# Performance work log

Hardware: AMD Instinct MI355X
Metric: run time of the kernel (lower is better)

## Reference

```python
import math
import jax
import jax.numpy as jnp
import numpy as np

N_IMG = 8
A = 3
H = 100
W = 100
STRIDE = 16
IMG = 1600
PRE_NMS_TOP_N = 2000
POST_NMS_TOP_N = 1000
NMS_THRESH = 0.7
MIN_SIZE = 0
BBOX_XFORM_CLIP = math.log(1000.0 / 16.0)


def setup_inputs() -> dict:
    key = jax.random.key(0)
    k1, k2 = jax.random.split(key)
    objectness = jax.random.normal(k1, (N_IMG, A, H, W), jnp.float32)
    box_regression = jax.random.normal(k2, (N_IMG, A * 4, H, W), jnp.float32) * 0.5
    # Grid anchors, flattened in (H, W, A) order to match objectness.permute(0,2,3,1)
    cy = (jnp.arange(H, dtype=jnp.float32) + 0.5) * STRIDE  # [H]
    cx = (jnp.arange(W, dtype=jnp.float32) + 0.5) * STRIDE  # [W]
    half = jnp.array([64.0, 128.0, 256.0], jnp.float32) / 2.0  # [A]
    cy = cy[:, None, None]  # [H,1,1]
    cx = cx[None, :, None]  # [1,W,1]
    s = half[None, None, :]  # [1,1,A]
    x1, y1, x2, y2 = jnp.broadcast_arrays(cx - s, cy - s, cx + s, cy + s)
    anc = jnp.stack([x1, y1, x2, y2], axis=-1).reshape(-1, 4)  # [H*W*A, 4]
    anchors = jnp.broadcast_to(anc[None], (N_IMG, H * W * A, 4)).copy()
    return {
        "objectness": objectness,
        "box_regression": box_regression,
        "anchors": anchors,
        "image_height": IMG,
        "image_width": IMG,
    }


def _decode(deltas, boxes):
    # BoxCoder(weights=(1,1,1,1)).decode with TO_REMOVE=1
    widths = boxes[..., 2] - boxes[..., 0] + 1.0
    heights = boxes[..., 3] - boxes[..., 1] + 1.0
    ctr_x = boxes[..., 0] + 0.5 * widths
    ctr_y = boxes[..., 1] + 0.5 * heights
    dx, dy = deltas[..., 0], deltas[..., 1]
    dw = jnp.minimum(deltas[..., 2], BBOX_XFORM_CLIP)
    dh = jnp.minimum(deltas[..., 3], BBOX_XFORM_CLIP)
    pcx = dx * widths + ctr_x
    pcy = dy * heights + ctr_y
    pw = jnp.exp(dw) * widths
    ph = jnp.exp(dh) * heights
    return jnp.stack(
        [pcx - 0.5 * pw, pcy - 0.5 * ph, pcx + 0.5 * pw - 1.0, pcy + 0.5 * ph - 1.0],
        axis=-1,
    )


def _nms_keep(boxes, valid, thresh):
    # boxes [n,4] sorted by descending score; valid: pre-filter mask.
    n = boxes.shape[0]
    x1, y1, x2, y2 = boxes[:, 0], boxes[:, 1], boxes[:, 2], boxes[:, 3]
    areas = (x2 - x1 + 1.0) * (y2 - y1 + 1.0)
    xx1 = jnp.maximum(x1[:, None], x1[None, :])
    yy1 = jnp.maximum(y1[:, None], y1[None, :])
    xx2 = jnp.minimum(x2[:, None], x2[None, :])
    yy2 = jnp.minimum(y2[:, None], y2[None, :])
    inter = jnp.maximum(xx2 - xx1 + 1.0, 0.0) * jnp.maximum(yy2 - yy1 + 1.0, 0.0)
    iou = inter / (areas[:, None] + areas[None, :] - inter)
    idx = jnp.arange(n)

    def body(i, keep):
        sup = keep[i] & (iou[i] > thresh) & (idx > i)
        return keep & ~sup

    return jax.lax.fori_loop(0, n, body, valid)


def _forward(objectness, box_regression, anchors, image_height, image_width):
    N, A_, H_, W_ = objectness.shape
    scores = jax.nn.sigmoid(objectness.transpose(0, 2, 3, 1).reshape(N, -1))  # [N, A*H*W]
    deltas = (
        box_regression.reshape(N, A_, 4, H_, W_)
        .transpose(0, 3, 4, 1, 2)
        .reshape(N, -1, 4)
    )
    pre = min(PRE_NMS_TOP_N, scores.shape[1])
    top_scores, top_idx = jax.lax.top_k(scores, pre)  # sorted descending
    deltas = jnp.take_along_axis(deltas, top_idx[:, :, None], axis=1)
    anc = jnp.take_along_axis(anchors, top_idx[:, :, None], axis=1)
    props = _decode(deltas, anc)  # [N, pre, 4]
    # clip to image (fact = 1)
    xs = jnp.clip(props[..., 0::2], 0.0, image_width - 1.0)
    ys = jnp.clip(props[..., 1::2], 0.0, image_height - 1.0)
    props = jnp.stack([xs[..., 0], ys[..., 0], xs[..., 1], ys[..., 1]], axis=-1)
    # filter small / out-of-image-center boxes
    ws = props[..., 2] - props[..., 0] + 1.0
    hs = props[..., 3] - props[..., 1] + 1.0
    xc = props[..., 0] + ws / 2.0
    yc = props[..., 1] + hs / 2.0
    valid = (ws >= MIN_SIZE) & (hs >= MIN_SIZE) & (xc < image_width) & (yc < image_height)
    keep = jax.vmap(lambda b, v: _nms_keep(b, v, NMS_THRESH))(props, valid)

    def _select(b, s, k):
        # compact kept boxes (already score-sorted) into fixed-size output
        rank = jnp.cumsum(k) - 1
        tgt = jnp.where(k & (rank < POST_NMS_TOP_N), rank, POST_NMS_TOP_N)
        ob = jnp.zeros((POST_NMS_TOP_N + 1, 4), b.dtype).at[tgt].set(b)[:POST_NMS_TOP_N]
        os = jnp.zeros((POST_NMS_TOP_N + 1,), s.dtype).at[tgt].set(s)[:POST_NMS_TOP_N]
        ov = jnp.arange(POST_NMS_TOP_N) < jnp.minimum(jnp.sum(k), POST_NMS_TOP_N)
        return ob, os, ov

    return jax.vmap(_select)(props, top_scores, keep)


def reference(objectness, box_regression, anchors, image_height, image_width):
    # Returns (boxes [N,post,4], objectness scores [N,post], valid mask [N,post])
    return _forward(objectness, box_regression, anchors, image_height, image_width)
```

## Files before the change

kernel.cpp:

```cpp
#include <hip/hip_runtime.h>
#include <math.h>
#include <stdint.h>

#define NIMG   8
#define NA     30000
#define PRE_N  2000
#define POST_N 1000
#define NMS_TH 0.7f
#define DCLIP  4.135166556742356f
#define IMGF   1600.0f
#define IMGM1  1599.0f
#define CAND_MAX 4096


__global__ __launch_bounds__(1024) void hist_compact(
    const float* __restrict__ obj,
    uint64_t* __restrict__ candBuf, unsigned int* __restrict__ candCnt)
{
    const int n    = blockIdx.x;
    const int tid  = threadIdx.x;
    const int lane = tid & 63;
    const int wid  = tid >> 6;

    __shared__ unsigned int hist[4096];
    __shared__ unsigned int wsum[16];
    __shared__ unsigned int scal[4];

    for (int b = tid; b < 4096; b += 1024) hist[b] = 0u;
    if (tid < 4) scal[tid] = 0u;
    __syncthreads();

    const float* objn = obj + n * NA;

    for (int j = tid; j < NA; j += 1024) {
        unsigned int u = __float_as_uint(objn[j]);
        unsigned int k = (u & 0x80000000u) ? ~u : (u | 0x80000000u);
        atomicAdd(&hist[k >> 20], 1u);
    }
    __syncthreads();

    unsigned int c0 = hist[tid*4+0], c1 = hist[tid*4+1],
                 c2 = hist[tid*4+2], c3 = hist[tid*4+3];
    unsigned int p = c0 + c1 + c2 + c3;
    unsigned int s = p;
    #pragma unroll
    for (int off = 1; off < 64; off <<= 1) {
        unsigned int v = __shfl_down(s, off);
        if (lane + off < 64) s += v;
    }
    if (lane == 0) wsum[wid] = s;
    __syncthreads();
    unsigned int wafter = 0;
    for (int w = wid + 1; w < 16; ++w) wafter += wsum[w];
    unsigned int after = (s - p) + wafter;
    {
        unsigned int S3 = after + c3;
        unsigned int S2 = S3 + c2;
        unsigned int S1 = S2 + c1;
        unsigned int S0 = S1 + c0;
        if (S3 >= PRE_N && after < PRE_N) { scal[2] = tid*4+3; }
        if (S2 >= PRE_N && S3    < PRE_N) { scal[2] = tid*4+2; }
        if (S1 >= PRE_N && S2    < PRE_N) { scal[2] = tid*4+1; }
        if (S0 >= PRE_N && S1    < PRE_N) { scal[2] = tid*4+0; }
    }
    __syncthreads();
    const unsigned int bstar = scal[2];

    for (int j = tid; j < NA; j += 1024) {
        unsigned int u = __float_as_uint(objn[j]);
        unsigned int k = (u & 0x80000000u) ? ~u : (u | 0x80000000u);
        if ((k >> 20) < bstar) continue;
        int a = j / 10000, t = j - a * 10000;
        uint64_t key = (((uint64_t)(~k)) << 32) | (unsigned int)(t * 3 + a);
        unsigned int pos = atomicAdd(&scal[0], 1u);
        if (pos < CAND_MAX) candBuf[n * CAND_MAX + pos] = key;
    }
    __syncthreads();
    if (tid == 0) candCnt[n] = min(scal[0], (unsigned int)CAND_MAX);
}

__global__ __launch_bounds__(64) void rank_decode(
    const float* __restrict__ breg,
    const uint64_t* __restrict__ candBuf, const unsigned int* __restrict__ candCnt,
    float* __restrict__ wsBoxes, float* __restrict__ wsScores,
    int* __restrict__ wsValid)
{
    const int n    = blockIdx.x >> 6;
    const int tile = blockIdx.x & 63;
    const int lane = threadIdx.x;

    const int C = (int)candCnt[n];
    if (tile * 64 >= C) return;

    const uint64_t* cb = candBuf + n * CAND_MAX;
    const int my = tile * 64 + lane;
    const uint64_t km = (my < C) ? cb[my] : ~0ull;

    unsigned int rank = 0;
    const int nch = (C + 63) >> 6;
    for (int ch = 0; ch < nch; ++ch) {
        const int j = ch * 64 + lane;
        uint64_t ck = (j < C) ? cb[j] : ~0ull;
        unsigned int clo = (unsigned int)ck, chi = (unsigned int)(ck >> 32);
        #pragma unroll
        for (int c = 0; c < 64; ++c) {
            unsigned int lo = (unsigned int)__builtin_amdgcn_readlane((int)clo, c);
            unsigned int hi = (unsigned int)__builtin_amdgcn_readlane((int)chi, c);
            uint64_t kc = ((uint64_t)hi << 32) | lo;
            rank += (kc < km) ? 1u : 0u;
        }
    }
    if (my >= C || rank >= PRE_N) return;

    unsigned int idx = (unsigned int)km;
    unsigned int k   = ~((unsigned int)(km >> 32));
    unsigned int u   = (k & 0x80000000u) ? (k & 0x7fffffffu) : ~k;
    float logit = __uint_as_float(u);
    float score = 1.0f / (1.0f + expf(-logit));

    int a = idx % 3, t = idx / 3, w = t % 100, h = t / 100;
    const float* bp = breg + n*120000 + (a*4)*10000 + t;
    float dx = bp[0], dy = bp[10000], dw = bp[20000], dh = bp[30000];

    float half = (a == 0) ? 32.0f : ((a == 1) ? 64.0f : 128.0f);
    float cx = w * 16.0f + 8.0f, cy = h * 16.0f + 8.0f;
    float x1 = cx - half, y1 = cy - half, x2 = cx + half, y2 = cy + half;
    float wd = x2 - x1 + 1.0f, hg = y2 - y1 + 1.0f;
    float cxr = x1 + 0.5f * wd, cyr = y1 + 0.5f * hg;
    dw = fminf(dw, DCLIP); dh = fminf(dh, DCLIP);
    float pcx = dx * wd + cxr, pcy = dy * hg + cyr;
    float pw = expf(dw) * wd, ph = expf(dh) * hg;
    float px1 = pcx - 0.5f * pw, py1 = pcy - 0.5f * ph;
    float px2 = pcx + 0.5f * pw - 1.0f, py2 = pcy + 0.5f * ph - 1.0f;
    px1 = fminf(fmaxf(px1, 0.0f), IMGM1);
    px2 = fminf(fmaxf(px2, 0.0f), IMGM1);
    py1 = fminf(fmaxf(py1, 0.0f), IMGM1);
    py2 = fminf(fmaxf(py2, 0.0f), IMGM1);
    float wss = px2 - px1 + 1.0f, hss = py2 - py1 + 1.0f;
    float xc = px1 + wss * 0.5f, yc = py1 + hss * 0.5f;
    int valid = (wss >= 0.0f) && (hss >= 0.0f) && (xc < IMGF) && (yc < IMGF);

    ((float4*)wsBoxes)[n * PRE_N + (int)rank] = make_float4(px1, py1, px2, py2);
    wsScores[n * PRE_N + (int)rank] = score;
    wsValid [n * PRE_N + (int)rank] = valid;
}

__global__ __launch_bounds__(512) void nms_mask(
    const float* __restrict__ wsBoxes, uint64_t* __restrict__ mask)
{
    const int blk  = blockIdx.x;
    const int n    = blk >> 5;
    const int i_t  = blk & 31;
    const int tid  = threadIdx.x;
    const int lane = tid & 63;
    const int wv   = tid >> 6;

    __shared__ uint64_t tile[64 * 33];

    for (int idx = tid; idx < 64 * 33; idx += 512) tile[idx] = 0ull;
    __syncthreads();

    const int r = i_t * 64 + lane;
    float4 rb = (r < PRE_N) ? ((const float4*)wsBoxes)[n * PRE_N + r]
                            : make_float4(0.f, 0.f, 0.f, 0.f);
    float ra = (rb.z - rb.x + 1.0f) * (rb.w - rb.y + 1.0f);

    for (int j_t = i_t + wv; j_t < 32; j_t += 8) {
        const int j = j_t * 64 + lane;
        float4 cb = (j < PRE_N) ? ((const float4*)wsBoxes)[n * PRE_N + j]
                                : make_float4(3e30f, 3e30f, 3e30f, 3e30f);
        float ca = (cb.z - cb.x + 1.0f) * (cb.w - cb.y + 1.0f);
        const uint64_t jmask = (j_t == 31) ? 0xFFFFull : ~0ull;
        const bool diag = (j_t == i_t);
        uint64_t myword = 0ull;

        #pragma unroll
        for (int c = 0; c < 64; ++c) {
            float rx1 = __int_as_float(__builtin_amdgcn_readlane(__float_as_int(rb.x), c));
            float ry1 = __int_as_float(__builtin_amdgcn_readlane(__float_as_int(rb.y), c));
            float rx2 = __int_as_float(__builtin_amdgcn_readlane(__float_as_int(rb.z), c));
            float ry2 = __int_as_float(__builtin_amdgcn_readlane(__float_as_int(rb.w), c));
            float rar = __int_as_float(__builtin_amdgcn_readlane(__float_as_int(ra), c));
            float xx1 = fmaxf(rx1, cb.x), yy1 = fmaxf(ry1, cb.y);
            float xx2 = fminf(rx2, cb.z), yy2 = fminf(ry2, cb.w);
            float ww = fmaxf(xx2 - xx1 + 1.0f, 0.0f);
            float hh = fmaxf(yy2 - yy1 + 1.0f, 0.0f);
            float inter = ww * hh;
            float denom = rar + ca - inter;
            unsigned long long bits = __ballot(inter > NMS_TH * denom) & jmask;
            if (diag) bits &= (c == 63) ? 0ull : ((~0ull) << (c + 1));
            if (lane == c) myword = bits;
        }
        tile[lane * 33 + j_t] = myword;
    }
    __syncthreads();

    uint64_t* mrow = mask + ((size_t)n * PRE_N + (size_t)i_t * 64) * 32;
    const int cmax = (i_t == 31) ? 16 : 64;
    for (int idx = tid; idx < cmax * 32; idx += 512) {
        const int rr = idx >> 5, w = idx & 31;
        mrow[idx] = tile[rr * 33 + w];
    }
}

#define SL(n,b) \
    "global_load_dword v" #n ", %[voff], %[sbase]\n\t" \
    "v_add_u32 %[voff], 0x100, %[voff]\n\t"

#define SS(n,b) \
    "s_waitcnt vmcnt(63)\n\t" \
    "v_readlane_b32 %[t], v" #n ", %[lw]\n\t" \
    "s_bitcmp1_b32 %[win], " #b "\n\t" \
    "s_cselect_b32 %[m], 0, -1\n\t" \
    "s_sub_i32 %[kept], %[kept], %[m]\n\t" \
    "s_and_b32 %[t], %[t], %[m]\n\t" \
    "s_or_b32 %[win], %[win], %[t]\n\t" \
    "v_and_b32 v" #n ", %[m], v" #n "\n\t" \
    "v_or_b32 %[rem], %[rem], v" #n "\n\t" \
    "global_load_dword v" #n ", %[voff], %[sbase]\n\t" \
    "v_add_u32 %[voff], 0x100, %[voff]\n\t"

#define SN(n,b,w) \
    "s_waitcnt vmcnt(" #w ")\n\t" \
    "v_readlane_b32 %[t], v" #n ", %[lw]\n\t" \
    "s_bitcmp1_b32 %[win], " #b "\n\t" \
    "s_cselect_b32 %[m], 0, -1\n\t" \
    "s_sub_i32 %[kept], %[kept], %[m]\n\t" \
    "s_and_b32 %[t], %[t], %[m]\n\t" \
    "s_or_b32 %[win], %[win], %[t]\n\t" \
    "v_and_b32 v" #n ", %[m], v" #n "\n\t" \
    "v_or_b32 %[rem], %[rem], v" #n "\n\t"

#define SWIN \
    "s_add_u32 %[lw], %[lw], 1\n\t" \
    "v_readlane_b32 %[t], %[rem], %[lw]\n\t" \
    "s_mov_b32 %[win], %[t]\n\t"

#define ROW_A(M) M(64,0) M(65,1) M(66,2) M(67,3) M(68,4) M(69,5) M(70,6) M(71,7) \
    M(72,8) M(73,9) M(74,10) M(75,11) M(76,12) M(77,13) M(78,14) M(79,15) \
    M(80,16) M(81,17) M(82,18) M(83,19) M(84,20) M(85,21) M(86,22) M(87,23) \
    M(88,24) M(89,25) M(90,26) M(91,27) M(92,28) M(93,29) M(94,30) M(95,31)
#define ROW_B(M) M(96,0) M(97,1) M(98,2) M(99,3) M(100,4) M(101,5) M(102,6) M(103,7) \
    M(104,8) M(105,9) M(106,10) M(107,11) M(108,12) M(109,13) M(110,14) M(111,15) \
    M(112,16) M(113,17) M(114,18) M(115,19) M(116,20) M(117,21) M(118,22) M(119,23) \
    M(120,24) M(121,25) M(122,26) M(123,27) M(124,28) M(125,29) M(126,30) M(127,31)

__global__ __launch_bounds__(256) void nms_scan_select(
    const float* __restrict__ wsBoxes, const float* __restrict__ wsScores,
    const int* __restrict__ wsValid, const uint64_t* __restrict__ mask,
    float* __restrict__ out)
{
    const int n   = blockIdx.x;
    const int tid = threadIdx.x;

    __shared__ __align__(8) unsigned char invb[256];
    __shared__ unsigned int keepw32[64];
    __shared__ int sscan[256];

    unsigned int byte = 0xFFu;
    if (tid < PRE_N / 8) {
        byte = 0u;
        for (int q = 0; q < 8; ++q)
            byte |= (wsValid[n * PRE_N + tid * 8 + q] ? 0u : 1u) << q;
    }
    invb[tid] = (unsigned char)byte;
    __syncthreads();

    if (tid < 64) {
        unsigned int rem = ((const unsigned int*)invb)[tid];
        unsigned long long sbase =
            (unsigned long long)(const void*)(mask + (size_t)n * PRE_N * 32);
        unsigned int voff = (unsigned int)(tid * 4);
        int win_, m_, t_, lw_, kept_, cnt_;

        asm volatile(
            "s_waitcnt vmcnt(0) lgkmcnt(0)\n\t"
            "s_mov_b32 %[kept], 0\n\t"
            "s_mov_b32 %[lw], 0\n\t"
            ROW_A(SL) ROW_B(SL)
            "v_readlane_b32 %[t], %[rem], %[lw]\n\t"
            "s_mov_b32 %[win], %[t]\n\t"
            "s_mov_b32 %[cnt], 30\n\t"
            "Lnms_%=:\n\t"
            ROW_A(SS)
            SWIN
            ROW_B(SS)
            SWIN
            "s_cmp_ge_i32 %[kept], 0x3e8\n\t"
            "s_cbranch_scc1 Lend_%=\n\t"
            "s_sub_u32 %[cnt], %[cnt], 1\n\t"
            "s_cmp_lg_u32 %[cnt], 0\n\t"
            "s_cbranch_scc1 Lnms_%=\n\t"
            SS(64,0) SS(65,1) SS(66,2) SS(67,3) SS(68,4) SS(69,5) SS(70,6) SS(71,7)
            SS(72,8) SS(73,9) SS(74,10) SS(75,11) SS(76,12) SS(77,13) SS(78,14) SS(79,15)
            SN(80,16,63) SN(81,17,62) SN(82,18,61) SN(83,19,60)
            SN(84,20,59) SN(85,21,58) SN(86,22,57) SN(87,23,56)
            SN(88,24,55) SN(89,25,54) SN(90,26,53) SN(91,27,52)
            SN(92,28,51) SN(93,29,50) SN(94,30,49) SN(95,31,48)
            SWIN
            SN(96,0,47) SN(97,1,46) SN(98,2,45) SN(99,3,44)
            SN(100,4,43) SN(101,5,42) SN(102,6,41) SN(103,7,40)
            SN(104,8,39) SN(105,9,38) SN(106,10,37) SN(107,11,36)
            SN(108,12,35) SN(109,13,34) SN(110,14,33) SN(111,15,32)
            SN(112,16,31) SN(113,17,30) SN(114,18,29) SN(115,19,28)
            SN(116,20,27) SN(117,21,26) SN(118,22,25) SN(119,23,24)
            SN(120,24,23) SN(121,25,22) SN(122,26,21) SN(123,27,20)
            SN(124,28,19) SN(125,29,18) SN(126,30,17) SN(127,31,16)
            SWIN
            SN(64,0,15) SN(65,1,14) SN(66,2,13) SN(67,3,12)
            SN(68,4,11) SN(69,5,10) SN(70,6,9) SN(71,7,8)
            SN(72,8,7) SN(73,9,6) SN(74,10,5) SN(75,11,4)
            SN(76,12,3) SN(77,13,2) SN(78,14,1) SN(79,15,0)
            "Lend_%=:\n\t"
            "s_waitcnt vmcnt(0)\n\t"
            : [rem]"+v"(rem), [voff]"+v"(voff),
              [win]"=&s"(win_), [m]"=&s"(m_), [t]"=&s"(t_),
              [lw]"=&s"(lw_), [kept]"=&s"(kept_), [cnt]"=&s"(cnt_)
            : [sbase]"s"(sbase)
            : "scc", "vcc", "memory",
              "v64","v65","v66","v67","v68","v69","v70","v71",
              "v72","v73","v74","v75","v76","v77","v78","v79",
              "v80","v81","v82","v83","v84","v85","v86","v87",
              "v88","v89","v90","v91","v92","v93","v94","v95",
              "v96","v97","v98","v99","v100","v101","v102","v103",
              "v104","v105","v106","v107","v108","v109","v110","v111",
              "v112","v113","v114","v115","v116","v117","v118","v119",
              "v120","v121","v122","v123","v124","v125","v126","v127");

        keepw32[tid] = ~rem;
    }
    __syncthreads();

    int c[8]; const int base8 = tid * 8;
    int lsum = 0;
    for (int q = 0; q < 8; ++q) {
        const int i = base8 + q;
        c[q] = (i < PRE_N) ? (int)((keepw32[i >> 5] >> (i & 31)) & 1u) : 0;
        lsum += c[q];
    }
    sscan[tid] = lsum;
    __syncthreads();
    for (int off = 1; off < 256; off <<= 1) {
        int v = (tid >= off) ? sscan[tid - off] : 0;
        __syncthreads();
        sscan[tid] += v;
        __syncthreads();
    }
    const int excl  = sscan[tid] - lsum;
    const int total = sscan[255];

    float* ob  = out + n * POST_N * 4;
    float* osc = out + NIMG * POST_N * 4 + n * POST_N;
    float* ovd = out + NIMG * POST_N * 5 + n * POST_N;

    for (int i = tid; i < POST_N * 4; i += 256) ob[i] = 0.0f;
    for (int i = tid; i < POST_N; i += 256) osc[i] = 0.0f;
    const int lim = min(total, POST_N);
    for (int i = tid; i < POST_N; i += 256) ovd[i] = (i < lim) ? 1.0f : 0.0f;
    __syncthreads();

    int run = excl;
    for (int q = 0; q < 8; ++q) {
        const int i = base8 + q;
        if (i < PRE_N && c[q]) {
            if (run < POST_N) {
                float4 b = ((const float4*)wsBoxes)[n * PRE_N + i];
                ob[run * 4 + 0] = b.x;
                ob[run * 4 + 1] = b.y;
                ob[run * 4 + 2] = b.z;
                ob[run * 4 + 3] = b.w;
                osc[run] = wsScores[n * PRE_N + i];
            }
            run++;
        }
    }
}

extern "C" void kernel_launch(void* const* d_in, const int* in_sizes, int n_in,
                              void* d_out, int out_size, void* d_ws, size_t ws_size,
                              hipStream_t stream) {
    const float* obj  = (const float*)d_in[0];
    const float* breg = (const float*)d_in[1];
    float* ws        = (float*)d_ws;
    float* wsBoxes   = ws;
    float* wsScores  = ws + 64000;
    int*   wsValid   = (int*)(ws + 80000);
    uint64_t* wsMask = (uint64_t*)(ws + 96000);
    uint64_t*     candBuf = wsMask;
    unsigned int* candCnt = (unsigned int*)(wsMask + NIMG * CAND_MAX);

    hist_compact<<<NIMG, 1024, 0, stream>>>(obj, candBuf, candCnt);
    rank_decode<<<NIMG * 64, 64, 0, stream>>>(breg, candBuf, candCnt,
                                              wsBoxes, wsScores, wsValid);
    nms_mask<<<NIMG * 32, 512, 0, stream>>>(wsBoxes, wsMask);
    nms_scan_select<<<NIMG, 256, 0, stream>>>(wsBoxes, wsScores, wsValid, wsMask,
                                              (float*)d_out);
}
```

Baseline: 185.0 us.

## Fuse top-k selection and decode into one kernel with bucketed ranking

Merges the histogram/compaction kernel and the rank/decode kernel into a single per-image kernel. Candidates are scattered into shared memory grouped by histogram bucket using suffix offsets, so each candidate's rank only needs comparisons within its own bucket instead of against all candidates. This removes a kernel launch, the global candidate buffer round trip, and the quadratic rank loop. In exchange, decode now runs on only 8 blocks, and large buckets could cause serial comparison loops.

```diff
diff --git a/kernel.cpp b/kernel.cpp
--- a/kernel.cpp
+++ b/kernel.cpp
@@ -13,21 +13,23 @@
 #define CAND_MAX 4096
 
 
-__global__ __launch_bounds__(1024) void hist_compact(
-    const float* __restrict__ obj,
-    uint64_t* __restrict__ candBuf, unsigned int* __restrict__ candCnt)
+__global__ __launch_bounds__(1024) void topk_decode(
+    const float* __restrict__ obj, const float* __restrict__ breg,
+    float* __restrict__ wsBoxes, float* __restrict__ wsScores,
+    int* __restrict__ wsValid)
 {
     const int n    = blockIdx.x;
     const int tid  = threadIdx.x;
     const int lane = tid & 63;
     const int wid  = tid >> 6;
 
-    __shared__ unsigned int hist[4096];
-    __shared__ unsigned int wsum[16];
-    __shared__ unsigned int scal[4];
+    __shared__ unsigned int   hist[4096];
+    __shared__ unsigned short sufx[4096];
+    __shared__ uint64_t       grp[CAND_MAX];
+    __shared__ unsigned int   wsum[16];
+    __shared__ unsigned int   sbstar;
 
     for (int b = tid; b < 4096; b += 1024) hist[b] = 0u;
-    if (tid < 4) scal[tid] = 0u;
     __syncthreads();
 
     const float* objn = obj + n * NA;
@@ -58,91 +60,79 @@
         unsigned int S2 = S3 + c2;
         unsigned int S1 = S2 + c1;
         unsigned int S0 = S1 + c0;
-        if (S3 >= PRE_N && after < PRE_N) { scal[2] = tid*4+3; }
-        if (S2 >= PRE_N && S3    < PRE_N) { scal[2] = tid*4+2; }
-        if (S1 >= PRE_N && S2    < PRE_N) { scal[2] = tid*4+1; }
-        if (S0 >= PRE_N && S1    < PRE_N) { scal[2] = tid*4+0; }
-    }
-    __syncthreads();
-    const unsigned int bstar = scal[2];
+        if (S3 >= PRE_N && after < PRE_N) { sbstar = tid*4+3; }
+        if (S2 >= PRE_N && S3    < PRE_N) { sbstar = tid*4+2; }
+        if (S1 >= PRE_N && S2    < PRE_N) { sbstar = tid*4+1; }
+        if (S0 >= PRE_N && S1    < PRE_N) { sbstar = tid*4+0; }
+        sufx[tid*4+0] = (unsigned short)S1;
+        sufx[tid*4+1] = (unsigned short)S2;
+        sufx[tid*4+2] = (unsigned short)S3;
+        sufx[tid*4+3] = (unsigned short)after;
+    }
+    hist[tid*4+0] = 0u; hist[tid*4+1] = 0u;
+    hist[tid*4+2] = 0u; hist[tid*4+3] = 0u;
+    __syncthreads();
+    const unsigned int bstar = sbstar;
 
     for (int j = tid; j < NA; j += 1024) {
         unsigned int u = __float_as_uint(objn[j]);
         unsigned int k = (u & 0x80000000u) ? ~u : (u | 0x80000000u);
-        if ((k >> 20) < bstar) continue;
+        unsigned int b = k >> 20;
+        if (b < bstar) continue;
         int a = j / 10000, t = j - a * 10000;
         uint64_t key = (((uint64_t)(~k)) << 32) | (unsigned int)(t * 3 + a);
-        unsigned int pos = atomicAdd(&scal[0], 1u);
-        if (pos < CAND_MAX) candBuf[n * CAND_MAX + pos] = key;
-    }
-    __syncthreads();
-    if (tid == 0) candCnt[n] = min(scal[0], (unsigned int)CAND_MAX);
-}
-
-__global__ __launch_bounds__(64) void rank_decode(
-    const float* __restrict__ breg,
-    const uint64_t* __restrict__ candBuf, const unsigned int* __restrict__ candCnt,
-    float* __restrict__ wsBoxes, float* __restrict__ wsScores,
-    int* __restrict__ wsValid)
-{
-    const int n    = blockIdx.x >> 6;
-    const int tile = blockIdx.x & 63;
-    const int lane = threadIdx.x;
-
-    const int C = (int)candCnt[n];
-    if (tile * 64 >= C) return;
-
-    const uint64_t* cb = candBuf + n * CAND_MAX;
-    const int my = tile * 64 + lane;
-    const uint64_t km = (my < C) ? cb[my] : ~0ull;
-
-    unsigned int rank = 0;
-    const int nch = (C + 63) >> 6;
-    for (int ch = 0; ch < nch; ++ch) {
-        const int j = ch * 64 + lane;
-        uint64_t ck = (j < C) ? cb[j] : ~0ull;
-        unsigned int clo = (unsigned int)ck, chi = (unsigned int)(ck >> 32);
-        #pragma unroll
-        for (int c = 0; c < 64; ++c) {
-            unsigned int lo = (unsigned int)__builtin_amdgcn_readlane((int)clo, c);
-            unsigned int hi = (unsigned int)__builtin_amdgcn_readlane((int)chi, c);
-            uint64_t kc = ((uint64_t)hi << 32) | lo;
-            rank += (kc < km) ? 1u : 0u;
-        }
-    }
-    if (my >= C || rank >= PRE_N) return;
-
-    unsigned int idx = (unsigned int)km;
-    unsigned int k   = ~((unsigned int)(km >> 32));
-    unsigned int u   = (k & 0x80000000u) ? (k & 0x7fffffffu) : ~k;
-    float logit = __uint_as_float(u);
-    float score = 1.0f / (1.0f + expf(-logit));
-
-    int a = idx % 3, t = idx / 3, w = t % 100, h = t / 100;
-    const float* bp = breg + n*120000 + (a*4)*10000 + t;
-    float dx = bp[0], dy = bp[10000], dw = bp[20000], dh = bp[30000];
-
-    float half = (a == 0) ? 32.0f : ((a == 1) ? 64.0f : 128.0f);
-    float cx = w * 16.0f + 8.0f, cy = h * 16.0f + 8.0f;
-    float x1 = cx - half, y1 = cy - half, x2 = cx + half, y2 = cy + half;
-    float wd = x2 - x1 + 1.0f, hg = y2 - y1 + 1.0f;
-    float cxr = x1 + 0.5f * wd, cyr = y1 + 0.5f * hg;
-    dw = fminf(dw, DCLIP); dh = fminf(dh, DCLIP);
-    float pcx = dx * wd + cxr, pcy = dy * hg + cyr;
-    float pw = expf(dw) * wd, ph = expf(dh) * hg;
-    float px1 = pcx - 0.5f * pw, py1 = pcy - 0.5f * ph;
-    float px2 = pcx + 0.5f * pw - 1.0f, py2 = pcy + 0.5f * ph - 1.0f;
-    px1 = fminf(fmaxf(px1, 0.0f), IMGM1);
-    px2 = fminf(fmaxf(px2, 0.0f), IMGM1);
-    py1 = fminf(fmaxf(py1, 0.0f), IMGM1);
-    py2 = fminf(fmaxf(py2, 0.0f), IMGM1);
-    float wss = px2 - px1 + 1.0f, hss = py2 - py1 + 1.0f;
-    float xc = px1 + wss * 0.5f, yc = py1 + hss * 0.5f;
-    int valid = (wss >= 0.0f) && (hss >= 0.0f) && (xc < IMGF) && (yc < IMGF);
-
-    ((float4*)wsBoxes)[n * PRE_N + (int)rank] = make_float4(px1, py1, px2, py2);
-    wsScores[n * PRE_N + (int)rank] = score;
-    wsValid [n * PRE_N + (int)rank] = valid;
+        unsigned int slot = (unsigned int)sufx[b] + atomicAdd(&hist[b], 1u);
+        if (slot < CAND_MAX) grp[slot] = key;
+    }
+    __syncthreads();
+
+    const unsigned int total =
+        min((unsigned int)sufx[bstar] + hist[bstar], (unsigned int)CAND_MAX);
+
+    for (unsigned int slot = tid; slot < total; slot += 1024) {
+        const uint64_t key = grp[slot];
+        const unsigned int hi = (unsigned int)(key >> 32);
+        const unsigned int b  = 4095u - (hi >> 20);
+        const unsigned int gbeg = sufx[b];
+        const unsigned int gend =
+            min(gbeg + hist[b], (unsigned int)CAND_MAX);
+        unsigned int rank = gbeg;
+        for (unsigned int g = gbeg; g < gend; ++g)
+            rank += (grp[g] < key) ? 1u : 0u;
+        if (rank >= PRE_N) continue;
+
+        unsigned int idx = (unsigned int)key;
+        unsigned int k   = ~hi;
+        unsigned int u   = (k & 0x80000000u) ? (k & 0x7fffffffu) : ~k;
+        float logit = __uint_as_float(u);
+        float score = 1.0f / (1.0f + expf(-logit));
+
+        int a = idx % 3, t = idx / 3, w = t % 100, h = t / 100;
+        const float* bp = breg + n*120000 + (a*4)*10000 + t;
+        float dx = bp[0], dy = bp[10000], dw = bp[20000], dh = bp[30000];
+
+        float half = (a == 0) ? 32.0f : ((a == 1) ? 64.0f : 128.0f);
+        float cx = w * 16.0f + 8.0f, cy = h * 16.0f + 8.0f;
+        float x1 = cx - half, y1 = cy - half, x2 = cx + half, y2 = cy + half;
+        float wd = x2 - x1 + 1.0f, hg = y2 - y1 + 1.0f;
+        float cxr = x1 + 0.5f * wd, cyr = y1 + 0.5f * hg;
+        dw = fminf(dw, DCLIP); dh = fminf(dh, DCLIP);
+        float pcx = dx * wd + cxr, pcy = dy * hg + cyr;
+        float pw = expf(dw) * wd, ph = expf(dh) * hg;
+        float px1 = pcx - 0.5f * pw, py1 = pcy - 0.5f * ph;
+        float px2 = pcx + 0.5f * pw - 1.0f, py2 = pcy + 0.5f * ph - 1.0f;
+        px1 = fminf(fmaxf(px1, 0.0f), IMGM1);
+        px2 = fminf(fmaxf(px2, 0.0f), IMGM1);
+        py1 = fminf(fmaxf(py1, 0.0f), IMGM1);
+        py2 = fminf(fmaxf(py2, 0.0f), IMGM1);
+        float wss = px2 - px1 + 1.0f, hss = py2 - py1 + 1.0f;
+        float xc = px1 + wss * 0.5f, yc = py1 + hss * 0.5f;
+        int valid = (wss >= 0.0f) && (hss >= 0.0f) && (xc < IMGF) && (yc < IMGF);
+
+        ((float4*)wsBoxes)[n * PRE_N + (int)rank] = make_float4(px1, py1, px2, py2);
+        wsScores[n * PRE_N + (int)rank] = score;
+        wsValid [n * PRE_N + (int)rank] = valid;
+    }
 }
 
 __global__ __launch_bounds__(512) void nms_mask(
@@ -386,12 +376,8 @@
     float* wsScores  = ws + 64000;
     int*   wsValid   = (int*)(ws + 80000);
     uint64_t* wsMask = (uint64_t*)(ws + 96000);
-    uint64_t*     candBuf = wsMask;
-    unsigned int* candCnt = (unsigned int*)(wsMask + NIMG * CAND_MAX);
-
-    hist_compact<<<NIMG, 1024, 0, stream>>>(obj, candBuf, candCnt);
-    rank_decode<<<NIMG * 64, 64, 0, stream>>>(breg, candBuf, candCnt,
-                                              wsBoxes, wsScores, wsValid);
+
+    topk_decode<<<NIMG, 1024, 0, stream>>>(obj, breg, wsBoxes, wsScores, wsValid);
     nms_mask<<<NIMG * 32, 512, 0, stream>>>(wsBoxes, wsMask);
     nms_scan_select<<<NIMG, 256, 0, stream>>>(wsBoxes, wsScores, wsValid, wsMask,
                                               (float*)d_out);
```

After: 210.5 us. +13.8%, slower.
